# Kernel optimization log

Hardware: AMD Instinct MI355X
Metric: run time of the kernel (lower is better)

Reference implementation:

```python
import jax, jax.numpy as jnp
import numpy as np

B, S, E, H = 2, 2048, 1024, 16
D = E // H


def setup_inputs() -> dict:
    key = jax.random.key(0)
    ks = jax.random.split(key, 8)
    hidden_states = jax.random.normal(ks[0], (B, S, E), dtype=jnp.float32)
    # q/k/v projections: small random init
    Wq = jax.random.normal(ks[1], (E, E), dtype=jnp.float32) * 0.02
    Wk = jax.random.normal(ks[2], (E, E), dtype=jnp.float32) * 0.02
    Wv = jax.random.normal(ks[3], (E, E), dtype=jnp.float32) * 0.02
    bq = jnp.zeros((E,), jnp.float32)
    bk = jnp.zeros((E,), jnp.float32)
    bv = jnp.zeros((E,), jnp.float32)
    # hedgehog feature maps: identity init (per init_weights_) + small noise
    eye = jnp.eye(E, dtype=jnp.float32)
    Wfq = eye + jax.random.normal(ks[4], (E, E), dtype=jnp.float32) * 0.02
    Wfk = eye + jax.random.normal(ks[5], (E, E), dtype=jnp.float32) * 0.02
    bfq = jnp.zeros((E,), jnp.float32)
    bfk = jnp.zeros((E,), jnp.float32)
    return dict(hidden_states=hidden_states, Wq=Wq, bq=bq, Wk=Wk, bk=bk,
                Wv=Wv, bv=bv, Wfq=Wfq, bfq=bfq, Wfk=Wfk, bfk=bfk)


def reference(hidden_states, Wq, bq, Wk, bk, Wv, bv, Wfq, bfq, Wfk, bfk):
    b, s, e = hidden_states.shape
    d = e // H
    # feature maps: linear -> linear -> softmax over full hidden dim (before head split)
    q = jax.nn.softmax((hidden_states @ Wq.T + bq) @ Wfq.T + bfq, axis=-1)
    k = jax.nn.softmax((hidden_states @ Wk.T + bk) @ Wfk.T + bfk, axis=-1)
    v = hidden_states @ Wv.T + bv
    split = lambda t: t.reshape(b, s, H, d).transpose(0, 2, 1, 3)  # [B,H,S,D]
    q, k, v = split(q), split(k), split(v)
    scores = jnp.einsum('bhsd,bhtd->bhst', q, k)          # [B,H,S,S], nonnegative
    probs = scores / jnp.sum(scores, axis=-1, keepdims=True)  # sum-normalization
    ctx = jnp.einsum('bhst,bhtd->bhsd', probs, v)
    return ctx.transpose(0, 2, 1, 3).reshape(b, s, e)
```

## Files before the change

kernel.cpp:

```cpp
#include <hip/hip_runtime.h>
#include <math.h>

constexpr int B = 2, S = 2048, E = 1024, H = 16, D = 64;
constexpr int M = B * S;
constexpr int CH = 16;

typedef __attribute__((ext_vector_type(8))) short short8;
typedef __attribute__((ext_vector_type(8))) _Float16 half8;
typedef __attribute__((ext_vector_type(4))) float f32x4;
#define MFMA_BF16 __builtin_amdgcn_mfma_f32_16x16x32_bf16
#define MFMA_F16 __builtin_amdgcn_mfma_f32_16x16x32_f16
#define WAITCNT_VM(N) __builtin_amdgcn_s_waitcnt(0xF70 | (N))

__device__ __forceinline__ void split1(float f, short* h, short* l) {
  unsigned u = __float_as_uint(f);
  *h = (short)(u >> 16);
  float r = f - __uint_as_float(u & 0xFFFF0000u);
  *l = (short)(__float_as_uint(r) >> 16);
}
__device__ __forceinline__ short f2h(float f) {
  _Float16 h = (_Float16)f;
  short s;
  __builtin_memcpy(&s, &h, 2);
  return s;
}
__device__ __forceinline__ float h2f(short s) {
  _Float16 h;
  __builtin_memcpy(&h, &s, 2);
  return (float)h;
}

__device__ __forceinline__ void gload16(const void* g, const void* l) {
  __builtin_amdgcn_global_load_lds(
      (const __attribute__((address_space(1))) unsigned*)g,
      (__attribute__((address_space(3))) unsigned*)l, 16, 0, 0);
}

struct SArgs {
  const short* Ah; const short* Al;
  const short* Bh; const short* Bl;
  const float* bias;
  float* C;
  short* Ch; short* Cl;
};
struct HArgs {
  const short* A; const short* Bm;
  const float* bias;
  short* C;
  float* Zrow;
};

template <int BM, int WEMIT>
__global__ __launch_bounds__(256, 2) void gemm_combo(SArgs s, HArgs ha, HArgs hb, int K, int N) {
  __shared__ short lds[(BM / 8 + 16) * 512];
  const int tid = threadIdx.x, wave = tid >> 6, lane = tid & 63;
  const int bm = blockIdx.x * BM, bn = blockIdx.y * 128;
  const int fr = lane & 15, fq = lane >> 4;
  const int wm = (wave & 1) * (BM / 2), wn = (wave >> 1) * 64;
  constexpr int MT = BM / 32;

  if (blockIdx.z == 0) {
    constexpr int SA = BM / 16;
    constexpr int TOT = 2 * SA + 16;
    constexpr int PW = TOT / 4;
    const short* gb[PW];
#pragma unroll
    for (int j = 0; j < PW; ++j) {
      const int n = wave * PW + j;
      const short* src; int seg, rowbase;
      if (n < SA)              { src = s.Ah; seg = n;            rowbase = bm; }
      else if (n < 2 * SA)     { src = s.Al; seg = n - SA;       rowbase = bm; }
      else if (n < 2 * SA + 8) { src = s.Bh; seg = n - 2 * SA;   rowbase = bn; }
      else                     { src = s.Bl; seg = n - 2 * SA - 8; rowbase = bn; }
      const int r = seg * 16 + (lane >> 2);
      const int p = lane & 3;
      const int q = (p - ((r >> 1) & 3)) & 3;
      gb[j] = src + (size_t)(rowbase + r) * K + q * 8;
    }
    int aoh[MT], aol[MT], boh[4], bol[4];
#pragma unroll
    for (int mi = 0; mi < MT; ++mi) {
      const int r = wm + mi * 16 + fr;
      const int slot = (fq + ((r >> 1) & 3)) & 3;
      aoh[mi] = r * 32 + slot * 8;
      aol[mi] = BM * 32 + aoh[mi];
    }
#pragma unroll
    for (int ni = 0; ni < 4; ++ni) {
      const int r = wn + ni * 16 + fr;
      const int slot = (fq + ((r >> 1) & 3)) & 3;
      boh[ni] = 2 * BM * 32 + r * 32 + slot * 8;
      bol[ni] = boh[ni] + 4096;
    }
    f32x4 acc[MT][4] = {};
    const int ldsW = wave * PW * 512;
    for (int k0 = 0; k0 < K; k0 += 32) {
#pragma unroll
      for (int j = 0; j < PW; ++j) gload16(gb[j] + k0, &lds[ldsW + j * 512]);
      __syncthreads();
      short8 ah[MT], al[MT], bh4[4], bl4[4];
#pragma unroll
      for (int mi = 0; mi < MT; ++mi) {
        ah[mi] = *(const short8*)&lds[aoh[mi]];
        al[mi] = *(const short8*)&lds[aol[mi]];
      }
#pragma unroll
      for (int ni = 0; ni < 4; ++ni) {
        bh4[ni] = *(const short8*)&lds[boh[ni]];
        bl4[ni] = *(const short8*)&lds[bol[ni]];
      }
#pragma unroll
      for (int mi = 0; mi < MT; ++mi)
#pragma unroll
        for (int ni = 0; ni < 4; ++ni) {
          acc[mi][ni] = MFMA_BF16(ah[mi], bh4[ni], acc[mi][ni], 0, 0, 0);
          acc[mi][ni] = MFMA_BF16(ah[mi], bl4[ni], acc[mi][ni], 0, 0, 0);
          acc[mi][ni] = MFMA_BF16(al[mi], bh4[ni], acc[mi][ni], 0, 0, 0);
        }
      __syncthreads();
    }
    if (WEMIT == 0) {
      float* C = s.C;
#pragma unroll
      for (int ni = 0; ni < 4; ++ni) {
        const int n = bn + wn + ni * 16 + fr;
        const float bv = s.bias[n];
#pragma unroll
        for (int mi = 0; mi < MT; ++mi) {
          const int m0 = bm + wm + mi * 16 + fq * 4;
#pragma unroll
          for (int r2 = 0; r2 < 4; ++r2)
            C[(size_t)(m0 + r2) * N + n] = acc[mi][ni][r2] + bv;
        }
      }
    } else {
      short* Chp = s.Ch; short* Clp = s.Cl;
#pragma unroll
      for (int ni = 0; ni < 4; ++ni) {
        const int n = bn + wn + ni * 16 + fr;
#pragma unroll
        for (int mi = 0; mi < MT; ++mi) {
          const int m0 = bm + wm + mi * 16 + fq * 4;
#pragma unroll
          for (int r2 = 0; r2 < 4; ++r2) {
            short hh, ll;
            split1(acc[mi][ni][r2], &hh, &ll);
            Chp[(size_t)(m0 + r2) * N + n] = hh;
            Clp[(size_t)(m0 + r2) * N + n] = ll;
          }
        }
      }
    }
    return;
  }

  const HArgs h = (blockIdx.z == 1) ? ha : hb;
  constexpr int SAh = BM / 16;
  constexpr int TOTh = SAh + 8;
  constexpr int PWh = TOTh / 4;
  const short* gb[PWh];
#pragma unroll
  for (int j = 0; j < PWh; ++j) {
    const int n = wave * PWh + j;
    const short* src; int seg, rowbase;
    if (n < SAh) { src = h.A;  seg = n;       rowbase = bm; }
    else         { src = h.Bm; seg = n - SAh; rowbase = bn; }
    const int r = seg * 16 + (lane >> 2);
    const int p = lane & 3;
    const int q = (p - ((r >> 1) & 3)) & 3;
    gb[j] = src + (size_t)(rowbase + r) * K + q * 8;
  }
  int ao[MT], bo[4];
#pragma unroll
  for (int mi = 0; mi < MT; ++mi) {
    const int r = wm + mi * 16 + fr;
    ao[mi] = r * 32 + (((fq + ((r >> 1) & 3)) & 3)) * 8;
  }
#pragma unroll
  for (int ni = 0; ni < 4; ++ni) {
    const int r = wn + ni * 16 + fr;
    bo[ni] = BM * 32 + r * 32 + (((fq + ((r >> 1) & 3)) & 3)) * 8;
  }
  f32x4 acc[MT][4] = {};
  const int ldsW = wave * PWh * 512;
  auto stageAll = [&](int buf, int k0) {
#pragma unroll
    for (int j = 0; j < PWh; ++j)
      gload16(gb[j] + k0, &lds[buf * TOTh * 512 + ldsW + j * 512]);
  };
  stageAll(0, 0);
  stageAll(1, 32);
  int buf = 0;
  for (int k0 = 0; k0 < K; k0 += 32) {
    if (k0 + 32 < K) WAITCNT_VM(PWh); else WAITCNT_VM(0);
    __builtin_amdgcn_s_barrier();
    half8 ah[MT], bh4[4];
    const int bb = buf * TOTh * 512;
#pragma unroll
    for (int mi = 0; mi < MT; ++mi) ah[mi] = *(const half8*)&lds[bb + ao[mi]];
#pragma unroll
    for (int ni = 0; ni < 4; ++ni) bh4[ni] = *(const half8*)&lds[bb + bo[ni]];
#pragma unroll
    for (int mi = 0; mi < MT; ++mi)
#pragma unroll
      for (int ni = 0; ni < 4; ++ni)
        acc[mi][ni] = MFMA_F16(ah[mi], bh4[ni], acc[mi][ni], 0, 0, 0);
    __builtin_amdgcn_s_barrier();
    if (k0 + 64 < K) stageAll(buf, k0 + 64);
    buf ^= 1;
  }
  if (WEMIT == 0) {
    short* C = h.C;
    float bv4[4];
#pragma unroll
    for (int ni = 0; ni < 4; ++ni) bv4[ni] = h.bias[bn + wn + ni * 16 + fr];
#pragma unroll
    for (int mi = 0; mi < MT; ++mi)
#pragma unroll
      for (int r2 = 0; r2 < 4; ++r2) {
        const int m = bm + wm + mi * 16 + fq * 4 + r2;
        float vals[4];
#pragma unroll
        for (int ni = 0; ni < 4; ++ni) vals[ni] = acc[mi][ni][r2] + bv4[ni];
        if (h.Zrow) {
          float es = 0.f;
#pragma unroll
          for (int ni = 0; ni < 4; ++ni) { vals[ni] = __expf(vals[ni]); es += vals[ni]; }
#pragma unroll
          for (int off = 1; off < 16; off <<= 1) es += __shfl_xor(es, off, 16);
          if (fr == 0) atomicAdd(&h.Zrow[m], es);
        }
#pragma unroll
        for (int ni = 0; ni < 4; ++ni)
          C[(size_t)m * N + bn + wn + ni * 16 + fr] = f2h(vals[ni]);
      }
  } else {
    short* C = h.C;
#pragma unroll
    for (int ni = 0; ni < 4; ++ni) {
      const int n = bn + wn + ni * 16 + fr;
#pragma unroll
      for (int mi = 0; mi < MT; ++mi) {
        const int m0 = bm + wm + mi * 16 + fq * 4;
#pragma unroll
        for (int r2 = 0; r2 < 4; ++r2)
          C[(size_t)(m0 + r2) * N + n] = f2h(acc[mi][ni][r2]);
      }
    }
  }
}

__global__ __launch_bounds__(256) void prep(
    const float* __restrict__ hs, short* hs_h, short* hs_l, short* hs_f,
    const float* __restrict__ Wfq, short* Wfq_h, short* Wfq_l,
    const float* __restrict__ Wfk, short* Wfk_f,
    const float* __restrict__ Wv, short* Wv_f,
    const float* __restrict__ Wq, short* WqT_h, short* WqT_l,
    const float* __restrict__ Wk, short* WkT_f,
    const float* __restrict__ bq, const float* __restrict__ bfq, float* bcQ,
    const float* __restrict__ bk, const float* __restrict__ bfk, float* bcK) {
  __shared__ float tb[32][33];
  const int blk = blockIdx.x, tid = threadIdx.x;
  if (blk < 1024) {
#pragma unroll
    for (int p = 0; p < 4; ++p) {
      const int i = blk * 1024 + p * 256 + tid;
      float4 v = ((const float4*)hs)[i];
      short4 hh, ll;
      split1(v.x, &hh.x, &ll.x); split1(v.y, &hh.y, &ll.y);
      split1(v.z, &hh.z, &ll.z); split1(v.w, &hh.w, &ll.w);
      ((short4*)hs_h)[i] = hh; ((short4*)hs_l)[i] = ll;
      ((short4*)hs_f)[i] = make_short4(f2h(v.x), f2h(v.y), f2h(v.z), f2h(v.w));
    }
  } else if (blk < 1280) {
    const int base = blk - 1024;
#pragma unroll
    for (int p = 0; p < 4; ++p) {
      const int i = base * 1024 + p * 256 + tid;
      float4 v = ((const float4*)Wfq)[i];
      short4 hh, ll;
      split1(v.x, &hh.x, &ll.x); split1(v.y, &hh.y, &ll.y);
      split1(v.z, &hh.z, &ll.z); split1(v.w, &hh.w, &ll.w);
      ((short4*)Wfq_h)[i] = hh; ((short4*)Wfq_l)[i] = ll;
    }
  } else if (blk < 1792) {
    const int base = blk - 1280;
    const float* src = (base < 256) ? Wfk : Wv;
    short* dst = (base < 256) ? Wfk_f : Wv_f;
    const int bb = base & 255;
#pragma unroll
    for (int p = 0; p < 4; ++p) {
      const int i = bb * 1024 + p * 256 + tid;
      float4 v = ((const float4*)src)[i];
      ((short4*)dst)[i] = make_short4(f2h(v.x), f2h(v.y), f2h(v.z), f2h(v.w));
    }
  } else if (blk < 2816) {
    const int tt = blk - 1792;
    const int bx = (tt & 31) * 32, by = (tt >> 5) * 32;
    const int x = tid & 31, y0 = tid >> 5;
#pragma unroll
    for (int i = 0; i < 32; i += 8) tb[y0 + i][x] = Wq[(size_t)(by + y0 + i) * E + bx + x];
    __syncthreads();
#pragma unroll
    for (int i = 0; i < 32; i += 8) {
      short hh, ll;
      split1(tb[x][y0 + i], &hh, &ll);
      const size_t o = (size_t)(bx + y0 + i) * E + by + x;
      WqT_h[o] = hh; WqT_l[o] = ll;
    }
  } else if (blk < 3840) {
    const int tt = blk - 2816;
    const int bx = (tt & 31) * 32, by = (tt >> 5) * 32;
    const int x = tid & 31, y0 = tid >> 5;
#pragma unroll
    for (int i = 0; i < 32; i += 8) tb[y0 + i][x] = Wk[(size_t)(by + y0 + i) * E + bx + x];
    __syncthreads();
#pragma unroll
    for (int i = 0; i < 32; i += 8)
      WkT_f[(size_t)(bx + y0 + i) * E + by + x] = f2h(tb[x][y0 + i]);
  } else {
    const int t = blk - 3840;
    const float* Wf = (t < 256) ? Wfq : Wfk;
    const float* bin = (t < 256) ? bq : bk;
    const float* bf = (t < 256) ? bfq : bfk;
    float* o = (t < 256) ? bcQ : bcK;
    const int n = (t & 255) * 4 + (tid >> 6);
    const int lane = tid & 63;
    float sacc = 0.f;
    for (int j = lane; j < E; j += 64) sacc += Wf[(size_t)n * E + j] * bin[j];
#pragma unroll
    for (int off = 32; off; off >>= 1) sacc += __shfl_xor(sacc, off, 64);
    if (lane == 0) o[n] = sacc + bf[n];
  }
}

__global__ __launch_bounds__(256) void kv_part(const short* __restrict__ kh,
                                               const short* __restrict__ vh,
                                               const float* __restrict__ Zk,
                                               float* __restrict__ KVp,
                                               float* __restrict__ ksump) {
  const int bh = blockIdx.x;
  const int b = bh / H, h = bh % H;
  const int t0 = blockIdx.y * 128;
  const short* kbase = kh + (size_t)b * S * E + (size_t)h * D;
  const short* vbase = vh + (size_t)b * S * E + (size_t)h * D;
  __shared__ float ks[16][D];
  __shared__ float vs[16][D];
  __shared__ float invZs[128];
  const int tid = threadIdx.x;
  if (tid < 128) invZs[tid] = 1.0f / Zk[b * S + t0 + tid];
  const int a4 = tid & 15, b4 = tid >> 4;
  const int lt = tid >> 4, d4 = (tid & 15) * 4;
  float acc[4][4] = {};
  float ksm[4] = {};
  for (int ts = 0; ts < 128; ts += 16) {
    __syncthreads();
    const size_t roff = (size_t)(t0 + ts + lt) * E + d4;
    short4 k4 = *(const short4*)(kbase + roff);
    short4 v4 = *(const short4*)(vbase + roff);
    const float iz = invZs[ts + lt];
    ks[lt][d4 + 0] = h2f(k4.x) * iz; ks[lt][d4 + 1] = h2f(k4.y) * iz;
    ks[lt][d4 + 2] = h2f(k4.z) * iz; ks[lt][d4 + 3] = h2f(k4.w) * iz;
    vs[lt][d4 + 0] = h2f(v4.x); vs[lt][d4 + 1] = h2f(v4.y);
    vs[lt][d4 + 2] = h2f(v4.z); vs[lt][d4 + 3] = h2f(v4.w);
    __syncthreads();
#pragma unroll
    for (int tt = 0; tt < 16; ++tt) {
      float kk4[4], vv4[4];
#pragma unroll
      for (int i = 0; i < 4; ++i) kk4[i] = ks[tt][a4 * 4 + i];
#pragma unroll
      for (int j = 0; j < 4; ++j) vv4[j] = vs[tt][b4 * 4 + j];
#pragma unroll
      for (int i = 0; i < 4; ++i) {
        ksm[i] += kk4[i];
#pragma unroll
        for (int j = 0; j < 4; ++j) acc[i][j] = fmaf(kk4[i], vv4[j], acc[i][j]);
      }
    }
  }
  float* kvout = KVp + ((size_t)bh * CH + blockIdx.y) * 4096;
#pragma unroll
  for (int i = 0; i < 4; ++i)
    *(float4*)&kvout[(a4 * 4 + i) * 64 + b4 * 4] =
        make_float4(acc[i][0], acc[i][1], acc[i][2], acc[i][3]);
  if (b4 == 0)
    *(float4*)&ksump[((size_t)bh * CH + blockIdx.y) * 64 + a4 * 4] =
        make_float4(ksm[0], ksm[1], ksm[2], ksm[3]);
}

__global__ __launch_bounds__(256) void kv_reduce(const float* __restrict__ KVp,
                                                 const float* __restrict__ ksump,
                                                 float* __restrict__ KV,
                                                 float* __restrict__ ksum) {
  const int bh = blockIdx.x, tid = threadIdx.x;
  for (int i = tid; i < 1024; i += 256) {
    float4 s = make_float4(0.f, 0.f, 0.f, 0.f);
#pragma unroll
    for (int c = 0; c < CH; ++c) {
      float4 p = ((const float4*)(KVp + ((size_t)bh * CH + c) * 4096))[i];
      s.x += p.x; s.y += p.y; s.z += p.z; s.w += p.w;
    }
    ((float4*)(KV + (size_t)bh * 4096))[i] = s;
  }
  if (tid < 16) {
    float4 s = make_float4(0.f, 0.f, 0.f, 0.f);
#pragma unroll
    for (int c = 0; c < CH; ++c) {
      float4 p = ((const float4*)(ksump + ((size_t)bh * CH + c) * 64))[tid];
      s.x += p.x; s.y += p.y; s.z += p.z; s.w += p.w;
    }
    ((float4*)(ksum + bh * 64))[tid] = s;
  }
}

__global__ __launch_bounds__(256) void out_v6(const float* __restrict__ qf,
                                              const float* __restrict__ KV,
                                              const float* __restrict__ ksum,
                                              float* __restrict__ out) {
  const int bh = blockIdx.x;
  const int b = bh >> 4, h = bh & 15;
  __shared__ float KVs[64][64];
  __shared__ float kss[64];
  __shared__ float qs[4][4][64];
  const int tid = threadIdx.x, wave = tid >> 6, lane = tid & 63;
  const int r2 = lane >> 4, g = lane & 15;
  for (int i = tid; i < 1024; i += 256)
    ((float4*)KVs)[i] = ((const float4*)(KV + (size_t)bh * 4096))[i];
  if (tid < 64) kss[tid] = ksum[bh * 64 + tid];
  __syncthreads();
  const float4 ks4 = *(const float4*)&kss[g * 4];
  const int row0 = blockIdx.y * 64 + wave * 16;
#pragma unroll
  for (int it = 0; it < 4; ++it) {
    const int row = row0 + it * 4 + r2;
    const size_t rowoff = ((size_t)b * S + row) * E + h * 64;
    float4 u = *(const float4*)(qf + rowoff + g * 4);
    u.x = __expf(u.x); u.y = __expf(u.y); u.z = __expf(u.z); u.w = __expf(u.w);
    float dn = u.x * ks4.x + u.y * ks4.y + u.z * ks4.z + u.w * ks4.w;
#pragma unroll
    for (int off = 1; off < 16; off <<= 1) dn += __shfl_xor(dn, off, 16);
    *(float4*)&qs[wave][r2][g * 4] = u;
    __syncthreads();
    float nx = 0.f, ny = 0.f, nz = 0.f, nw = 0.f;
#pragma unroll
    for (int d = 0; d < 64; ++d) {
      const float qd = qs[wave][r2][d];
      const float4 kv = *(const float4*)&KVs[d][g * 4];
      nx = fmaf(qd, kv.x, nx); ny = fmaf(qd, kv.y, ny);
      nz = fmaf(qd, kv.z, nz); nw = fmaf(qd, kv.w, nw);
    }
    const float inv = 1.0f / dn;
    float4 o4 = make_float4(nx * inv, ny * inv, nz * inv, nw * inv);
    *(float4*)(out + rowoff + g * 4) = o4;
    __syncthreads();
  }
}

extern "C" void kernel_launch(void* const* d_in, const int* in_sizes, int n_in,
                              void* d_out, int out_size, void* d_ws, size_t ws_size,
                              hipStream_t stream) {
  const float* hs = (const float*)d_in[0];
  const float* Wq = (const float*)d_in[1];
  const float* bq = (const float*)d_in[2];
  const float* Wk = (const float*)d_in[3];
  const float* bk = (const float*)d_in[4];
  const float* Wv = (const float*)d_in[5];
  const float* bv = (const float*)d_in[6];
  const float* Wfq = (const float*)d_in[7];
  const float* bfq = (const float*)d_in[8];
  const float* Wfk = (const float*)d_in[9];
  const float* bfk = (const float*)d_in[10];
  float* out = (float*)d_out;

  const size_t MEG = 1024 * 1024;
  float* ws = (float*)d_ws;
  float* qf = ws;
  short* kh = (short*)(ws + 4 * MEG);
  short* vh = (short*)(ws + 6 * MEG);
  short* hs_h = (short*)(ws + 8 * MEG);
  short* hs_l = (short*)(ws + 10 * MEG);
  short* hs_f = (short*)(ws + 12 * MEG);
  short* Wfq_h = (short*)(ws + 14 * MEG);
  short* Wfq_l = (short*)(ws + 14 * MEG + 512 * 1024);
  short* WqT_h = (short*)(ws + 15 * MEG);
  short* WqT_l = (short*)(ws + 15 * MEG + 512 * 1024);
  short* Wfk_f = (short*)(ws + 16 * MEG);
  short* WkT_f = (short*)(ws + 16 * MEG + 512 * 1024);
  short* Wv_f = (short*)(ws + 17 * MEG);
  short* WcQ_h = (short*)(ws + 17 * MEG + 512 * 1024);
  short* WcQ_l = (short*)(ws + 18 * MEG);
  short* WcK_f = (short*)(ws + 18 * MEG + 512 * 1024);
  float* bcQ = ws + 19 * MEG;
  float* bcK = bcQ + 1024;
  float* Zk = bcK + 1024;
  float* KV = Zk + M;
  float* ksum = KV + 32 * 4096;
  float* KVp = (float*)hs_h;
  float* ksump = (float*)hs_l;

  hipMemsetAsync(Zk, 0, M * sizeof(float), stream);
  prep<<<4352, 256, 0, stream>>>(hs, hs_h, hs_l, hs_f,
                                 Wfq, Wfq_h, Wfq_l, Wfk, Wfk_f, Wv, Wv_f,
                                 Wq, WqT_h, WqT_l, Wk, WkT_f,
                                 bq, bfq, bcQ, bk, bfk, bcK);
  SArgs sw = {Wfq_h, Wfq_l, WqT_h, WqT_l, nullptr, nullptr, WcQ_h, WcQ_l};
  HArgs hw = {Wfk_f, WkT_f, nullptr, WcK_f, nullptr};
  gemm_combo<64, 1><<<dim3(16, 8, 2), 256, 0, stream>>>(sw, hw, hw, E, E);
  SArgs sb = {hs_h, hs_l, WcQ_h, WcQ_l, bcQ, qf, nullptr, nullptr};
  HArgs hk = {hs_f, WcK_f, bcK, kh, Zk};
  HArgs hv = {hs_f, Wv_f, bv, vh, nullptr};
  gemm_combo<128, 0><<<dim3(32, 8, 3), 256, 0, stream>>>(sb, hk, hv, E, E);
  kv_part<<<dim3(B * H, CH), 256, 0, stream>>>(kh, vh, Zk, KVp, ksump);
  kv_reduce<<<B * H, 256, 0, stream>>>(KVp, ksump, KV, ksum);
  out_v6<<<dim3(B * H, S / 64), 256, 0, stream>>>(qf, KV, ksum, out);
}
```

Measured before the change: 221.1 us.

## Drop split-bf16 Q path, use single fp16 GEMM with fused exp

Replaces the three-MFMA split-bf16 (hi/lo) path for the Q projection and the folded Q weight with plain fp16 GEMMs, so all branches share one double-buffered fp16 kernel. The exp of the Q logits is fused into the GEMM epilogue and stored as fp16, which shrinks what the output kernel reads from fp32 to fp16. The Zk memset is folded into the prep kernel and occupancy is raised to 3 blocks per CU. This cuts prep traffic, MFMA count and memory writes, at the cost of lower precision on the Q path, where exp of unnormalized logits in fp16 risks overflow or accuracy loss.

```diff
diff --git a/kernel.cpp b/kernel.cpp
--- a/kernel.cpp
+++ b/kernel.cpp
@@ -5,19 +5,11 @@
 constexpr int M = B * S;
 constexpr int CH = 16;
 
-typedef __attribute__((ext_vector_type(8))) short short8;
 typedef __attribute__((ext_vector_type(8))) _Float16 half8;
 typedef __attribute__((ext_vector_type(4))) float f32x4;
-#define MFMA_BF16 __builtin_amdgcn_mfma_f32_16x16x32_bf16
 #define MFMA_F16 __builtin_amdgcn_mfma_f32_16x16x32_f16
 #define WAITCNT_VM(N) __builtin_amdgcn_s_waitcnt(0xF70 | (N))
 
-__device__ __forceinline__ void split1(float f, short* h, short* l) {
-  unsigned u = __float_as_uint(f);
-  *h = (short)(u >> 16);
-  float r = f - __uint_as_float(u & 0xFFFF0000u);
-  *l = (short)(__float_as_uint(r) >> 16);
-}
 __device__ __forceinline__ short f2h(float f) {
   _Float16 h = (_Float16)f;
   short s;
@@ -36,140 +28,42 @@
       (__attribute__((address_space(3))) unsigned*)l, 16, 0, 0);
 }
 
-struct SArgs {
-  const short* Ah; const short* Al;
-  const short* Bh; const short* Bl;
-  const float* bias;
-  float* C;
-  short* Ch; short* Cl;
-};
 struct HArgs {
-  const short* A; const short* Bm;
+  const short* A;
+  const short* Bm;
   const float* bias;
   short* C;
   float* Zrow;
+  int doExp;
 };
 
 template <int BM, int WEMIT>
-__global__ __launch_bounds__(256, 2) void gemm_combo(SArgs s, HArgs ha, HArgs hb, int K, int N) {
-  __shared__ short lds[(BM / 8 + 16) * 512];
+__global__ __launch_bounds__(256, 3) void gemmh(HArgs g0, HArgs g1, HArgs g2, int K, int N) {
+  const HArgs h = (blockIdx.z == 0) ? g0 : (blockIdx.z == 1 ? g1 : g2);
+  constexpr int SA = BM / 16;
+  constexpr int TOT = SA + 8;
+  constexpr int PW = TOT / 4;
+  constexpr int MT = BM / 32;
+  __shared__ short lds[2][TOT * 512];
+
   const int tid = threadIdx.x, wave = tid >> 6, lane = tid & 63;
   const int bm = blockIdx.x * BM, bn = blockIdx.y * 128;
-  const int fr = lane & 15, fq = lane >> 4;
-  const int wm = (wave & 1) * (BM / 2), wn = (wave >> 1) * 64;
-  constexpr int MT = BM / 32;
-
-  if (blockIdx.z == 0) {
-    constexpr int SA = BM / 16;
-    constexpr int TOT = 2 * SA + 16;
-    constexpr int PW = TOT / 4;
-    const short* gb[PW];
-#pragma unroll
-    for (int j = 0; j < PW; ++j) {
-      const int n = wave * PW + j;
-      const short* src; int seg, rowbase;
-      if (n < SA)              { src = s.Ah; seg = n;            rowbase = bm; }
-      else if (n < 2 * SA)     { src = s.Al; seg = n - SA;       rowbase = bm; }
-      else if (n < 2 * SA + 8) { src = s.Bh; seg = n - 2 * SA;   rowbase = bn; }
-      else                     { src = s.Bl; seg = n - 2 * SA - 8; rowbase = bn; }
-      const int r = seg * 16 + (lane >> 2);
-      const int p = lane & 3;
-      const int q = (p - ((r >> 1) & 3)) & 3;
-      gb[j] = src + (size_t)(rowbase + r) * K + q * 8;
-    }
-    int aoh[MT], aol[MT], boh[4], bol[4];
-#pragma unroll
-    for (int mi = 0; mi < MT; ++mi) {
-      const int r = wm + mi * 16 + fr;
-      const int slot = (fq + ((r >> 1) & 3)) & 3;
-      aoh[mi] = r * 32 + slot * 8;
-      aol[mi] = BM * 32 + aoh[mi];
-    }
-#pragma unroll
-    for (int ni = 0; ni < 4; ++ni) {
-      const int r = wn + ni * 16 + fr;
-      const int slot = (fq + ((r >> 1) & 3)) & 3;
-      boh[ni] = 2 * BM * 32 + r * 32 + slot * 8;
-      bol[ni] = boh[ni] + 4096;
-    }
-    f32x4 acc[MT][4] = {};
-    const int ldsW = wave * PW * 512;
-    for (int k0 = 0; k0 < K; k0 += 32) {
-#pragma unroll
-      for (int j = 0; j < PW; ++j) gload16(gb[j] + k0, &lds[ldsW + j * 512]);
-      __syncthreads();
-      short8 ah[MT], al[MT], bh4[4], bl4[4];
-#pragma unroll
-      for (int mi = 0; mi < MT; ++mi) {
-        ah[mi] = *(const short8*)&lds[aoh[mi]];
-        al[mi] = *(const short8*)&lds[aol[mi]];
-      }
-#pragma unroll
-      for (int ni = 0; ni < 4; ++ni) {
-        bh4[ni] = *(const short8*)&lds[boh[ni]];
-        bl4[ni] = *(const short8*)&lds[bol[ni]];
-      }
-#pragma unroll
-      for (int mi = 0; mi < MT; ++mi)
-#pragma unroll
-        for (int ni = 0; ni < 4; ++ni) {
-          acc[mi][ni] = MFMA_BF16(ah[mi], bh4[ni], acc[mi][ni], 0, 0, 0);
-          acc[mi][ni] = MFMA_BF16(ah[mi], bl4[ni], acc[mi][ni], 0, 0, 0);
-          acc[mi][ni] = MFMA_BF16(al[mi], bh4[ni], acc[mi][ni], 0, 0, 0);
-        }
-      __syncthreads();
-    }
-    if (WEMIT == 0) {
-      float* C = s.C;
-#pragma unroll
-      for (int ni = 0; ni < 4; ++ni) {
-        const int n = bn + wn + ni * 16 + fr;
-        const float bv = s.bias[n];
-#pragma unroll
-        for (int mi = 0; mi < MT; ++mi) {
-          const int m0 = bm + wm + mi * 16 + fq * 4;
-#pragma unroll
-          for (int r2 = 0; r2 < 4; ++r2)
-            C[(size_t)(m0 + r2) * N + n] = acc[mi][ni][r2] + bv;
-        }
-      }
-    } else {
-      short* Chp = s.Ch; short* Clp = s.Cl;
-#pragma unroll
-      for (int ni = 0; ni < 4; ++ni) {
-        const int n = bn + wn + ni * 16 + fr;
-#pragma unroll
-        for (int mi = 0; mi < MT; ++mi) {
-          const int m0 = bm + wm + mi * 16 + fq * 4;
-#pragma unroll
-          for (int r2 = 0; r2 < 4; ++r2) {
-            short hh, ll;
-            split1(acc[mi][ni][r2], &hh, &ll);
-            Chp[(size_t)(m0 + r2) * N + n] = hh;
-            Clp[(size_t)(m0 + r2) * N + n] = ll;
-          }
-        }
-      }
-    }
-    return;
-  }
-
-  const HArgs h = (blockIdx.z == 1) ? ha : hb;
-  constexpr int SAh = BM / 16;
-  constexpr int TOTh = SAh + 8;
-  constexpr int PWh = TOTh / 4;
-  const short* gb[PWh];
-#pragma unroll
-  for (int j = 0; j < PWh; ++j) {
-    const int n = wave * PWh + j;
+
+  const short* gb[PW];
+#pragma unroll
+  for (int j = 0; j < PW; ++j) {
+    const int n = wave * PW + j;
     const short* src; int seg, rowbase;
-    if (n < SAh) { src = h.A;  seg = n;       rowbase = bm; }
-    else         { src = h.Bm; seg = n - SAh; rowbase = bn; }
+    if (n < SA) { src = h.A;  seg = n;      rowbase = bm; }
+    else        { src = h.Bm; seg = n - SA; rowbase = bn; }
     const int r = seg * 16 + (lane >> 2);
     const int p = lane & 3;
     const int q = (p - ((r >> 1) & 3)) & 3;
     gb[j] = src + (size_t)(rowbase + r) * K + q * 8;
   }
+
+  const int fr = lane & 15, fq = lane >> 4;
+  const int wm = (wave & 1) * (BM / 2), wn = (wave >> 1) * 64;
   int ao[MT], bo[4];
 #pragma unroll
   for (int mi = 0; mi < MT; ++mi) {
@@ -181,25 +75,27 @@
     const int r = wn + ni * 16 + fr;
     bo[ni] = BM * 32 + r * 32 + (((fq + ((r >> 1) & 3)) & 3)) * 8;
   }
+
   f32x4 acc[MT][4] = {};
-  const int ldsW = wave * PWh * 512;
+  const int ldsW = wave * PW * 512;
+
   auto stageAll = [&](int buf, int k0) {
 #pragma unroll
-    for (int j = 0; j < PWh; ++j)
-      gload16(gb[j] + k0, &lds[buf * TOTh * 512 + ldsW + j * 512]);
+    for (int j = 0; j < PW; ++j)
+      gload16(gb[j] + k0, &lds[buf][ldsW + j * 512]);
   };
+
   stageAll(0, 0);
   stageAll(1, 32);
   int buf = 0;
   for (int k0 = 0; k0 < K; k0 += 32) {
-    if (k0 + 32 < K) WAITCNT_VM(PWh); else WAITCNT_VM(0);
+    if (k0 + 32 < K) WAITCNT_VM(PW); else WAITCNT_VM(0);
     __builtin_amdgcn_s_barrier();
     half8 ah[MT], bh4[4];
-    const int bb = buf * TOTh * 512;
-#pragma unroll
-    for (int mi = 0; mi < MT; ++mi) ah[mi] = *(const half8*)&lds[bb + ao[mi]];
-#pragma unroll
-    for (int ni = 0; ni < 4; ++ni) bh4[ni] = *(const half8*)&lds[bb + bo[ni]];
+#pragma unroll
+    for (int mi = 0; mi < MT; ++mi) ah[mi] = *(const half8*)&lds[buf][ao[mi]];
+#pragma unroll
+    for (int ni = 0; ni < 4; ++ni) bh4[ni] = *(const half8*)&lds[buf][bo[ni]];
 #pragma unroll
     for (int mi = 0; mi < MT; ++mi)
 #pragma unroll
@@ -209,6 +105,7 @@
     if (k0 + 64 < K) stageAll(buf, k0 + 64);
     buf ^= 1;
   }
+
   if (WEMIT == 0) {
     short* C = h.C;
     float bv4[4];
@@ -222,10 +119,12 @@
         float vals[4];
 #pragma unroll
         for (int ni = 0; ni < 4; ++ni) vals[ni] = acc[mi][ni][r2] + bv4[ni];
+        if (h.doExp) {
+#pragma unroll
+          for (int ni = 0; ni < 4; ++ni) vals[ni] = __expf(vals[ni]);
+        }
         if (h.Zrow) {
-          float es = 0.f;
-#pragma unroll
-          for (int ni = 0; ni < 4; ++ni) { vals[ni] = __expf(vals[ni]); es += vals[ni]; }
+          float es = vals[0] + vals[1] + vals[2] + vals[3];
 #pragma unroll
           for (int off = 1; off < 16; off <<= 1) es += __shfl_xor(es, off, 16);
           if (fr == 0) atomicAdd(&h.Zrow[m], es);
@@ -251,14 +150,15 @@
 }
 
 __global__ __launch_bounds__(256) void prep(
-    const float* __restrict__ hs, short* hs_h, short* hs_l, short* hs_f,
-    const float* __restrict__ Wfq, short* Wfq_h, short* Wfq_l,
+    const float* __restrict__ hs, short* hs_f,
+    const float* __restrict__ Wfq, short* Wfq_f,
     const float* __restrict__ Wfk, short* Wfk_f,
     const float* __restrict__ Wv, short* Wv_f,
-    const float* __restrict__ Wq, short* WqT_h, short* WqT_l,
+    const float* __restrict__ Wq, short* WqT_f,
     const float* __restrict__ Wk, short* WkT_f,
     const float* __restrict__ bq, const float* __restrict__ bfq, float* bcQ,
-    const float* __restrict__ bk, const float* __restrict__ bfk, float* bcK) {
+    const float* __restrict__ bk, const float* __restrict__ bfk, float* bcK,
+    float* Zk) {
   __shared__ float tb[32][33];
   const int blk = blockIdx.x, tid = threadIdx.x;
   if (blk < 1024) {
@@ -266,27 +166,12 @@
     for (int p = 0; p < 4; ++p) {
       const int i = blk * 1024 + p * 256 + tid;
       float4 v = ((const float4*)hs)[i];
-      short4 hh, ll;
-      split1(v.x, &hh.x, &ll.x); split1(v.y, &hh.y, &ll.y);
-      split1(v.z, &hh.z, &ll.z); split1(v.w, &hh.w, &ll.w);
-      ((short4*)hs_h)[i] = hh; ((short4*)hs_l)[i] = ll;
       ((short4*)hs_f)[i] = make_short4(f2h(v.x), f2h(v.y), f2h(v.z), f2h(v.w));
     }
-  } else if (blk < 1280) {
+  } else if (blk < 1792) {
     const int base = blk - 1024;
-#pragma unroll
-    for (int p = 0; p < 4; ++p) {
-      const int i = base * 1024 + p * 256 + tid;
-      float4 v = ((const float4*)Wfq)[i];
-      short4 hh, ll;
-      split1(v.x, &hh.x, &ll.x); split1(v.y, &hh.y, &ll.y);
-      split1(v.z, &hh.z, &ll.z); split1(v.w, &hh.w, &ll.w);
-      ((short4*)Wfq_h)[i] = hh; ((short4*)Wfq_l)[i] = ll;
-    }
-  } else if (blk < 1792) {
-    const int base = blk - 1280;
-    const float* src = (base < 256) ? Wfk : Wv;
-    short* dst = (base < 256) ? Wfk_f : Wv_f;
+    const float* src = (base < 256) ? Wfq : (base < 512 ? Wfk : Wv);
+    short* dst = (base < 256) ? Wfq_f : (base < 512 ? Wfk_f : Wv_f);
     const int bb = base & 255;
 #pragma unroll
     for (int p = 0; p < 4; ++p) {
@@ -294,31 +179,20 @@
       float4 v = ((const float4*)src)[i];
       ((short4*)dst)[i] = make_short4(f2h(v.x), f2h(v.y), f2h(v.z), f2h(v.w));
     }
-  } else if (blk < 2816) {
-    const int tt = blk - 1792;
+  } else if (blk < 3840) {
+    const int t = blk - 1792;
+    const float* in = (t < 1024) ? Wq : Wk;
+    short* oh = (t < 1024) ? WqT_f : WkT_f;
+    const int tt = t & 1023;
     const int bx = (tt & 31) * 32, by = (tt >> 5) * 32;
     const int x = tid & 31, y0 = tid >> 5;
 #pragma unroll
-    for (int i = 0; i < 32; i += 8) tb[y0 + i][x] = Wq[(size_t)(by + y0 + i) * E + bx + x];
-    __syncthreads();
-#pragma unroll
-    for (int i = 0; i < 32; i += 8) {
-      short hh, ll;
-      split1(tb[x][y0 + i], &hh, &ll);
-      const size_t o = (size_t)(bx + y0 + i) * E + by + x;
-      WqT_h[o] = hh; WqT_l[o] = ll;
-    }
-  } else if (blk < 3840) {
-    const int tt = blk - 2816;
-    const int bx = (tt & 31) * 32, by = (tt >> 5) * 32;
-    const int x = tid & 31, y0 = tid >> 5;
-#pragma unroll
-    for (int i = 0; i < 32; i += 8) tb[y0 + i][x] = Wk[(size_t)(by + y0 + i) * E + bx + x];
+    for (int i = 0; i < 32; i += 8) tb[y0 + i][x] = in[(size_t)(by + y0 + i) * E + bx + x];
     __syncthreads();
 #pragma unroll
     for (int i = 0; i < 32; i += 8)
-      WkT_f[(size_t)(bx + y0 + i) * E + by + x] = f2h(tb[x][y0 + i]);
-  } else {
+      oh[(size_t)(bx + y0 + i) * E + by + x] = f2h(tb[x][y0 + i]);
+  } else if (blk < 4352) {
     const int t = blk - 3840;
     const float* Wf = (t < 256) ? Wfq : Wfk;
     const float* bin = (t < 256) ? bq : bk;
@@ -331,6 +205,10 @@
 #pragma unroll
     for (int off = 32; off; off >>= 1) sacc += __shfl_xor(sacc, off, 64);
     if (lane == 0) o[n] = sacc + bf[n];
+  } else {
+#pragma unroll
+    for (int p = 0; p < 4; ++p)
+      ((float4*)Zk)[p * 256 + tid] = make_float4(0.f, 0.f, 0.f, 0.f);
   }
 }
 
@@ -414,7 +292,7 @@
   }
 }
 
-__global__ __launch_bounds__(256) void out_v6(const float* __restrict__ qf,
+__global__ __launch_bounds__(256) void out_v7(const short* __restrict__ uh,
                                               const float* __restrict__ KV,
                                               const float* __restrict__ ksum,
                                               float* __restrict__ out) {
@@ -435,8 +313,8 @@
   for (int it = 0; it < 4; ++it) {
     const int row = row0 + it * 4 + r2;
     const size_t rowoff = ((size_t)b * S + row) * E + h * 64;
-    float4 u = *(const float4*)(qf + rowoff + g * 4);
-    u.x = __expf(u.x); u.y = __expf(u.y); u.z = __expf(u.z); u.w = __expf(u.w);
+    short4 us = *(const short4*)(uh + rowoff + g * 4);
+    float4 u = make_float4(h2f(us.x), h2f(us.y), h2f(us.z), h2f(us.w));
     float dn = u.x * ks4.x + u.y * ks4.y + u.z * ks4.z + u.w * ks4.w;
 #pragma unroll
     for (int off = 1; off < 16; off <<= 1) dn += __shfl_xor(dn, off, 16);
@@ -475,43 +353,36 @@
 
   const size_t MEG = 1024 * 1024;
   float* ws = (float*)d_ws;
-  float* qf = ws;
-  short* kh = (short*)(ws + 4 * MEG);
-  short* vh = (short*)(ws + 6 * MEG);
-  short* hs_h = (short*)(ws + 8 * MEG);
-  short* hs_l = (short*)(ws + 10 * MEG);
-  short* hs_f = (short*)(ws + 12 * MEG);
-  short* Wfq_h = (short*)(ws + 14 * MEG);
-  short* Wfq_l = (short*)(ws + 14 * MEG + 512 * 1024);
-  short* WqT_h = (short*)(ws + 15 * MEG);
-  short* WqT_l = (short*)(ws + 15 * MEG + 512 * 1024);
-  short* Wfk_f = (short*)(ws + 16 * MEG);
-  short* WkT_f = (short*)(ws + 16 * MEG + 512 * 1024);
-  short* Wv_f = (short*)(ws + 17 * MEG);
-  short* WcQ_h = (short*)(ws + 17 * MEG + 512 * 1024);
-  short* WcQ_l = (short*)(ws + 18 * MEG);
-  short* WcK_f = (short*)(ws + 18 * MEG + 512 * 1024);
-  float* bcQ = ws + 19 * MEG;
+  short* uh = (short*)ws;
+  short* kh = (short*)(ws + 2 * MEG);
+  short* vh = (short*)(ws + 4 * MEG);
+  short* hs_f = (short*)(ws + 6 * MEG);
+  short* Wfq_f = (short*)(ws + 8 * MEG);
+  short* Wfk_f = (short*)(ws + 8 * MEG + 512 * 1024);
+  short* Wv_f = (short*)(ws + 9 * MEG);
+  short* WqT_f = (short*)(ws + 9 * MEG + 512 * 1024);
+  short* WkT_f = (short*)(ws + 10 * MEG);
+  short* WcQ_f = (short*)(ws + 10 * MEG + 512 * 1024);
+  short* WcK_f = (short*)(ws + 11 * MEG);
+  float* bcQ = ws + 12 * MEG;
   float* bcK = bcQ + 1024;
   float* Zk = bcK + 1024;
   float* KV = Zk + M;
   float* ksum = KV + 32 * 4096;
-  float* KVp = (float*)hs_h;
-  float* ksump = (float*)hs_l;
-
-  hipMemsetAsync(Zk, 0, M * sizeof(float), stream);
-  prep<<<4352, 256, 0, stream>>>(hs, hs_h, hs_l, hs_f,
-                                 Wfq, Wfq_h, Wfq_l, Wfk, Wfk_f, Wv, Wv_f,
-                                 Wq, WqT_h, WqT_l, Wk, WkT_f,
-                                 bq, bfq, bcQ, bk, bfk, bcK);
-  SArgs sw = {Wfq_h, Wfq_l, WqT_h, WqT_l, nullptr, nullptr, WcQ_h, WcQ_l};
-  HArgs hw = {Wfk_f, WkT_f, nullptr, WcK_f, nullptr};
-  gemm_combo<64, 1><<<dim3(16, 8, 2), 256, 0, stream>>>(sw, hw, hw, E, E);
-  SArgs sb = {hs_h, hs_l, WcQ_h, WcQ_l, bcQ, qf, nullptr, nullptr};
-  HArgs hk = {hs_f, WcK_f, bcK, kh, Zk};
-  HArgs hv = {hs_f, Wv_f, bv, vh, nullptr};
-  gemm_combo<128, 0><<<dim3(32, 8, 3), 256, 0, stream>>>(sb, hk, hv, E, E);
+  float* KVp = (float*)hs_f;
+  float* ksump = (float*)Wfq_f;
+
+  prep<<<4353, 256, 0, stream>>>(hs, hs_f, Wfq, Wfq_f, Wfk, Wfk_f, Wv, Wv_f,
+                                 Wq, WqT_f, Wk, WkT_f,
+                                 bq, bfq, bcQ, bk, bfk, bcK, Zk);
+  HArgs w0 = {Wfq_f, WqT_f, nullptr, WcQ_f, nullptr, 0};
+  HArgs w1 = {Wfk_f, WkT_f, nullptr, WcK_f, nullptr, 0};
+  gemmh<64, 1><<<dim3(16, 8, 2), 256, 0, stream>>>(w0, w1, w1, E, E);
+  HArgs gq = {hs_f, WcQ_f, bcQ, uh, nullptr, 1};
+  HArgs gk = {hs_f, WcK_f, bcK, kh, Zk, 1};
+  HArgs gv = {hs_f, Wv_f, bv, vh, nullptr, 0};
+  gemmh<128, 0><<<dim3(32, 8, 3), 256, 0, stream>>>(gq, gk, gv, E, E);
   kv_part<<<dim3(B * H, CH), 256, 0, stream>>>(kh, vh, Zk, KVp, ksump);
   kv_reduce<<<B * H, 256, 0, stream>>>(KVp, ksump, KV, ksum);
-  out_v6<<<dim3(B * H, S / 64), 256, 0, stream>>>(qf, KV, ksum, out);
-}
+  out_v7<<<dim3(B * H, S / 64), 256, 0, stream>>>(uh, KV, ksum, out);
+}
```

New measurement: 189.0 us. 14.5% less time.
